# Optimization experiments

Hardware: AMD Instinct MI355X
Metric: run time of the kernel (lower is better)

The kernel has to match this reference:

```python
import jax, jax.numpy as jnp
import numpy as np
from functools import partial

V_TH = 1.0            # cfg['init_v_th']
ATAN_ALPHA = 2.0      # default alpha of spikingjelly ATan surrogate

@jax.custom_vjp
def heaviside_atan(u):
    # forward: hard spike; backward: ATan surrogate gradient
    return (u > 0).astype(u.dtype)

def _hs_fwd(u):
    return (u > 0).astype(u.dtype), u

def _hs_bwd(u, g):
    s = (jnp.pi / 2.0) * ATAN_ALPHA * u
    return (g * (ATAN_ALPHA / 2.0) / (1.0 + s * s),)

heaviside_atan.defvjp(_hs_fwd, _hs_bwd)

def setup_inputs() -> dict:
    key = jax.random.key(0)
    T, B, C, H, W = 16, 32, 128, 32, 32
    x = jax.random.normal(key, (T, B, C, H, W), dtype=jnp.float32)
    return {"x": x}

def reference(x):
    # PLIF forward: per-timestep charge (v += x_t), fire (heaviside with ATan
    # surrogate), soft reset (v -= spike * v_th). Fused into a single scan so
    # the membrane state v stays resident across the time loop.
    def step(v, xt):
        v = v + xt                      # neuronal_charge
        spike = heaviside_atan(v - V_TH)  # neuronal_fire
        v = v - spike * V_TH            # soft_reset
        return v, spike

    v0 = jnp.zeros(x.shape[1:], dtype=x.dtype)  # [B, C, H, W]
    _, out = jax.lax.scan(step, v0, x)          # out: [T, B, C, H, W]
    return out
```

## Files before the change

kernel.cpp:

```cpp
#include <hip/hip_runtime.h>
#include <hip/hip_bf16.h>


#ifndef PLIF_T
#define PLIF_T 16
#endif

typedef float f32x4 __attribute__((ext_vector_type(4)));

__global__ __launch_bounds__(256) void plif_fwd_kernel(
    const f32x4* __restrict__ x, f32x4* __restrict__ out, int n4) {
    int i = blockIdx.x * blockDim.x + threadIdx.x;
    if (i >= n4) return;

    f32x4 xt[PLIF_T];
    #pragma unroll
    for (int t = 0; t < PLIF_T; ++t) {
        xt[t] = __builtin_nontemporal_load(&x[(size_t)t * (size_t)n4 + (size_t)i]);
    }

    f32x4 v = (f32x4)(0.f, 0.f, 0.f, 0.f);
    #pragma unroll
    for (int t = 0; t < PLIF_T; ++t) {
        v += xt[t];

        f32x4 s;
        s.x = (v.x > 1.0f) ? 1.0f : 0.0f;
        s.y = (v.y > 1.0f) ? 1.0f : 0.0f;
        s.z = (v.z > 1.0f) ? 1.0f : 0.0f;
        s.w = (v.w > 1.0f) ? 1.0f : 0.0f;

        v -= s;

        __builtin_nontemporal_store(s, &out[(size_t)t * (size_t)n4 + (size_t)i]);
    }
}

extern "C" void kernel_launch(void* const* d_in, const int* in_sizes, int n_in,
                              void* d_out, int out_size, void* d_ws, size_t ws_size,
                              hipStream_t stream) {
    const float* x = (const float*)d_in[0];
    float* out = (float*)d_out;

    const int total = in_sizes[0];
    const int n = total / PLIF_T;
    const int n4 = n / 4;

    const int block = 256;
    const int grid = (n4 + block - 1) / block;

    plif_fwd_kernel<<<grid, block, 0, stream>>>(
        (const f32x4*)x, (f32x4*)out, n4);
}
```

Measured before the change: 447.0 us.

## Add software-pipelined grid-stride PLIF kernel with double-buffered time loads

Introduces a kernel where each thread processes several spatial positions in a grid-stride loop, splitting the 16 timesteps into two halves loaded into alternating register buffers so loads for the next half or next position overlap compute and stores of the current one. The grid shrinks fourfold. Loads switch from nontemporal to regular loads. A fallback simple kernel handles sizes not divisible by the chunk.

```diff
diff --git a/kernel.cpp b/kernel.cpp
--- a/kernel.cpp
+++ b/kernel.cpp
@@ -8,30 +8,82 @@
 
 typedef float f32x4 __attribute__((ext_vector_type(4)));
 
-__global__ __launch_bounds__(256) void plif_fwd_kernel(
-    const f32x4* __restrict__ x, f32x4* __restrict__ out, int n4) {
-    int i = blockIdx.x * blockDim.x + threadIdx.x;
-    if (i >= n4) return;
+#define HALF_T 8
+#define ITERS 4
 
-    f32x4 xt[PLIF_T];
+__device__ __forceinline__ void plif_step8(f32x4& v, const f32x4* __restrict__ buf,
+                                           f32x4* __restrict__ out, size_t n4,
+                                           size_t i, int tbase) {
     #pragma unroll
-    for (int t = 0; t < PLIF_T; ++t) {
-        xt[t] = __builtin_nontemporal_load(&x[(size_t)t * (size_t)n4 + (size_t)i]);
-    }
-
-    f32x4 v = (f32x4)(0.f, 0.f, 0.f, 0.f);
-    #pragma unroll
-    for (int t = 0; t < PLIF_T; ++t) {
-        v += xt[t];
-
+    for (int k = 0; k < HALF_T; ++k) {
+        f32x4 xt = buf[k];
+        v += xt;
         f32x4 s;
         s.x = (v.x > 1.0f) ? 1.0f : 0.0f;
         s.y = (v.y > 1.0f) ? 1.0f : 0.0f;
         s.z = (v.z > 1.0f) ? 1.0f : 0.0f;
         s.w = (v.w > 1.0f) ? 1.0f : 0.0f;
+        v -= s;
+        __builtin_nontemporal_store(s, &out[(size_t)(tbase + k) * n4 + i]);
+    }
+}
 
+__device__ __forceinline__ void load8(f32x4* __restrict__ buf,
+                                      const f32x4* __restrict__ x, size_t n4,
+                                      size_t i, int tbase) {
+    #pragma unroll
+    for (int k = 0; k < HALF_T; ++k) {
+        buf[k] = x[(size_t)(tbase + k) * n4 + i];
+    }
+}
+
+__global__ __launch_bounds__(256) void plif_fwd_pipelined(
+    const f32x4* __restrict__ x, f32x4* __restrict__ out, int n4_i) {
+    const size_t n4 = (size_t)n4_i;
+    const size_t stride = (size_t)gridDim.x * blockDim.x;
+    size_t i = (size_t)blockIdx.x * blockDim.x + threadIdx.x;
+
+    f32x4 bufA[HALF_T];
+    f32x4 bufB[HALF_T];
+
+    load8(bufA, x, n4, i, 0);
+
+    #pragma unroll
+    for (int it = 0; it < ITERS - 1; ++it) {
+        f32x4 v = (f32x4)(0.f, 0.f, 0.f, 0.f);
+        load8(bufB, x, n4, i, HALF_T);
+        plif_step8(v, bufA, out, n4, i, 0);
+        load8(bufA, x, n4, i + stride, 0);
+        plif_step8(v, bufB, out, n4, i, HALF_T);
+        i += stride;
+    }
+
+    {
+        f32x4 v = (f32x4)(0.f, 0.f, 0.f, 0.f);
+        load8(bufB, x, n4, i, HALF_T);
+        plif_step8(v, bufA, out, n4, i, 0);
+        plif_step8(v, bufB, out, n4, i, HALF_T);
+    }
+}
+
+__global__ __launch_bounds__(256) void plif_fwd_simple(
+    const f32x4* __restrict__ x, f32x4* __restrict__ out, int n4) {
+    int i = blockIdx.x * blockDim.x + threadIdx.x;
+    if (i >= n4) return;
+    f32x4 xt[PLIF_T];
+    #pragma unroll
+    for (int t = 0; t < PLIF_T; ++t)
+        xt[t] = x[(size_t)t * (size_t)n4 + (size_t)i];
+    f32x4 v = (f32x4)(0.f, 0.f, 0.f, 0.f);
+    #pragma unroll
+    for (int t = 0; t < PLIF_T; ++t) {
+        v += xt[t];
+        f32x4 s;
+        s.x = (v.x > 1.0f) ? 1.0f : 0.0f;
+        s.y = (v.y > 1.0f) ? 1.0f : 0.0f;
+        s.z = (v.z > 1.0f) ? 1.0f : 0.0f;
+        s.w = (v.w > 1.0f) ? 1.0f : 0.0f;
         v -= s;
-
         __builtin_nontemporal_store(s, &out[(size_t)t * (size_t)n4 + (size_t)i]);
     }
 }
@@ -47,8 +99,15 @@
     const int n4 = n / 4;
 
     const int block = 256;
-    const int grid = (n4 + block - 1) / block;
+    const int chunk = block * ITERS;
 
-    plif_fwd_kernel<<<grid, block, 0, stream>>>(
-        (const f32x4*)x, (f32x4*)out, n4);
+    if (n4 % chunk == 0) {
+        const int grid = n4 / chunk;
+        plif_fwd_pipelined<<<grid, block, 0, stream>>>(
+            (const f32x4*)x, (f32x4*)out, n4);
+    } else {
+        const int grid = (n4 + block - 1) / block;
+        plif_fwd_simple<<<grid, block, 0, stream>>>(
+            (const f32x4*)x, (f32x4*)out, n4);
+    }
 }
```

Result: slower. 479.0 us (+7.2%).
